# Performance work log

Hardware: AMD Instinct MI355X
Metric: run time of the kernel (lower is better)

The kernel has to match this reference:

```python
import jax, jax.numpy as jnp
import numpy as np

N, C = 8, 3
HD, WD = 1024, 1280   # camera (depth) resolution
HS, WS = 800, 1280    # projector pattern resolution


def _build_calib():
    fx, fy, dx, dy = 1200.0, 1200.0, 640.0, 512.0
    ww = np.arange(WD, dtype=np.float32)[None, :].repeat(HD, 0)
    hh = np.arange(HD, dtype=np.float32)[:, None].repeat(WD, 1)
    vec = np.stack([(ww - dx) / fx, (hh - dy) / fy, np.ones_like(ww)], axis=2)  # [H,W,3]
    th = 0.15
    ext_rot = np.array([[np.cos(th), 0.0, np.sin(th)],
                        [0.0, 1.0, 0.0],
                        [-np.sin(th), 0.0, np.cos(th)]], np.float32)
    abc = np.einsum('ij,hwj->hwi', ext_rot, vec).astype(np.float32)  # [H,W,3]
    abc_mat = np.transpose(abc, (2, 0, 1))  # [3,H,W] (plb.a2t HWC->CHW)
    ext_tran = np.array([200.0, 0.0, 50.0], np.float32)
    pat_intrin = np.array([1100.0, 1100.0, 640.0, 400.0], np.float32)
    return abc_mat, ext_tran, pat_intrin


def setup_inputs() -> dict:
    key = jax.random.key(0)
    k1, k2 = jax.random.split(key)
    abc, tr, pi = _build_calib()
    depth_mat = 500.0 + 500.0 * jax.random.uniform(k1, (N, 1, HD, WD), jnp.float32)
    src_mat = jax.random.normal(k2, (N, C, HS, WS), jnp.float32)
    return {"depth_mat": depth_mat, "src_mat": src_mat,
            "abc_mat": jnp.asarray(abc), "ext_tran": jnp.asarray(tr),
            "pat_intrin": jnp.asarray(pi)}


def _grid_sample_border(src, gx, gy):
    # src: [N,C,Hs,Ws]; gx,gy: [N,H,W] normalized grid; bilinear,
    # align_corners=False, padding_mode='border' (torch semantics).
    n, c, hs, ws = src.shape
    x = ((gx + 1.0) * ws - 1.0) * 0.5
    y = ((gy + 1.0) * hs - 1.0) * 0.5
    x = jnp.clip(x, 0.0, ws - 1.0)
    y = jnp.clip(y, 0.0, hs - 1.0)
    x0 = jnp.floor(x)
    y0 = jnp.floor(y)
    wx = x - x0
    wy = y - y0
    x0i = x0.astype(jnp.int32)
    y0i = y0.astype(jnp.int32)
    x1i = jnp.minimum(x0i + 1, ws - 1)
    y1i = jnp.minimum(y0i + 1, hs - 1)
    b = jnp.arange(n)[:, None, None]

    def g(yi, xi):
        return src[b, :, yi, xi]  # [N,H,W,C]

    out = (g(y0i, x0i) * ((1.0 - wy) * (1.0 - wx))[..., None]
           + g(y0i, x1i) * ((1.0 - wy) * wx)[..., None]
           + g(y1i, x0i) * (wy * (1.0 - wx))[..., None]
           + g(y1i, x1i) * (wy * wx)[..., None])
    return jnp.transpose(out, (0, 3, 1, 2))  # [N,C,H,W]


def reference(depth_mat, src_mat, abc_mat, ext_tran, pat_intrin):
    hs, ws = src_mat.shape[-2:]
    denom = abc_mat[2] * depth_mat + ext_tran[2]          # [N,1,H,W]
    xx = (abc_mat[0] * depth_mat + ext_tran[0]) / denom
    yy = (abc_mat[1] * depth_mat + ext_tran[1]) / denom
    fu, fv, du, dv = pat_intrin
    uu = fu * xx + du
    vv = fv * yy + dv
    # NOTE: original normalizes by (size-1) even with align_corners=False;
    # replicated faithfully.
    gx = 2.0 * uu[:, 0] / (ws - 1) - 1.0                  # [N,H,W]
    gy = 2.0 * vv[:, 0] / (hs - 1) - 1.0
    return _grid_sample_border(src_mat, gx, gy)
```

## Files before the change

### kernel.cpp

```cpp
#include <hip/hip_runtime.h>

#define N_  8
#define C_  3
#define HD_ 1024
#define WD_ 1280
#define HS_ 800
#define WS_ 1280

typedef _Float16 h2_t __attribute__((ext_vector_type(2)));
typedef float f32x4 __attribute__((ext_vector_type(4)));

__device__ __forceinline__ unsigned pack_h2(float a, float b) {
    h2_t h;
    h.x = (_Float16)a;
    h.y = (_Float16)b;
    return __builtin_bit_cast(unsigned, h);
}
__device__ __forceinline__ h2_t as_h2(unsigned u) {
    return __builtin_bit_cast(h2_t, u);
}
__device__ __forceinline__ float fdot2(h2_t a, h2_t b, float c) {
#if __has_builtin(__builtin_amdgcn_fdot2)
    return __builtin_amdgcn_fdot2(a, b, c, false);
#else
    return (float)a.x * (float)b.x + (float)a.y * (float)b.y + c;
#endif
}

__global__ __launch_bounds__(256) void pair_pack_kernel(
    const float* __restrict__ src, uint4* __restrict__ ws)
{
    const size_t HWs = (size_t)HS_ * WS_;
    size_t g = (size_t)blockIdx.x * blockDim.x + threadIdx.x;
    if (g >= (size_t)N_ * HWs) return;
    int n = (int)(g / HWs);
    size_t p = g - (size_t)n * HWs;
    int x = (int)(p % WS_);
    int dx = (x < WS_ - 1) ? 1 : 0;

    const float* s0 = src + (size_t)n * C_ * HWs + p;
    const float* s1 = s0 + HWs;
    const float* s2 = s1 + HWs;

    float c0a = s0[0], c0b = s0[dx];
    float c1a = s1[0], c1b = s1[dx];
    float c2a = s2[0], c2b = s2[dx];

    uint4 e;
    e.x = pack_h2(c0a, c0b);
    e.y = pack_h2(c1a, c1b);
    e.z = pack_h2(c2a, c2b);
    e.w = 0u;
    ws[g] = e;
}

__global__ __launch_bounds__(256) void warp_main4_kernel(
    const float* __restrict__ depth,
    const uint4* __restrict__ wsrc,
    const float* __restrict__ abc,
    const float* __restrict__ tr,
    const float* __restrict__ pin,
    float* __restrict__ out)
{
    const int HW = HD_ * WD_;
    int t = blockIdx.x * blockDim.x + threadIdx.x;
    int base = t * 4;
    if (base >= N_ * HW) return;

    int n  = base / HW;
    int hw = base - n * HW;

    f32x4 d4 = *(const f32x4*)(depth + base);
    f32x4 a4 = *(const f32x4*)(abc + hw);
    f32x4 b4 = *(const f32x4*)(abc + HW + hw);
    f32x4 c4 = *(const f32x4*)(abc + 2 * HW + hw);

    float tx = tr[0], ty = tr[1], tz = tr[2];
    float fu = pin[0], fv = pin[1], du = pin[2], dv = pin[3];

    const size_t HWs = (size_t)HS_ * WS_;
    const uint4* sn = wsrc + (size_t)n * HWs;

    f32x4 r0, r1, r2;

#pragma unroll
    for (int i = 0; i < 4; ++i) {
        float d = d4[i];
        float a = a4[i];
        float b = b4[i];
        float c = c4[i];

        float denom = c * d + tz;
        float inv = 1.0f / denom;
        float xx = (a * d + tx) * inv;
        float yy = (b * d + ty) * inv;
        float uu = fu * xx + du;
        float vv = fv * yy + dv;

        float gx = 2.0f * uu / (float)(WS_ - 1) - 1.0f;
        float gy = 2.0f * vv / (float)(HS_ - 1) - 1.0f;
        float x = ((gx + 1.0f) * (float)WS_ - 1.0f) * 0.5f;
        float y = ((gy + 1.0f) * (float)HS_ - 1.0f) * 0.5f;

        x = fminf(fmaxf(x, 0.0f), (float)(WS_ - 1));
        y = fminf(fmaxf(y, 0.0f), (float)(HS_ - 1));

        float x0f = floorf(x);
        float y0f = floorf(y);
        float wx = x - x0f;
        float wy = y - y0f;
        int x0 = (int)x0f;
        int y0 = (int)y0f;
        int y1 = min(y0 + 1, HS_ - 1);

        uint4 E0 = sn[(size_t)y0 * WS_ + x0];
        uint4 E1 = sn[(size_t)y1 * WS_ + x0];

        float w00 = (1.0f - wy) * (1.0f - wx);
        float w01 = (1.0f - wy) * wx;
        float w10 = wy * (1.0f - wx);
        float w11 = wy * wx;

        h2_t wA = { (_Float16)w00, (_Float16)w01 };
        h2_t wB = { (_Float16)w10, (_Float16)w11 };

        r0[i] = fdot2(as_h2(E0.x), wA, fdot2(as_h2(E1.x), wB, 0.0f));
        r1[i] = fdot2(as_h2(E0.y), wA, fdot2(as_h2(E1.y), wB, 0.0f));
        r2[i] = fdot2(as_h2(E0.z), wA, fdot2(as_h2(E1.z), wB, 0.0f));
    }

    float* on = out + (size_t)n * C_ * HW + hw;
    __builtin_nontemporal_store(r0, (f32x4*)(on));
    __builtin_nontemporal_store(r1, (f32x4*)(on + (size_t)HW));
    __builtin_nontemporal_store(r2, (f32x4*)(on + (size_t)2 * HW));
}

__global__ __launch_bounds__(256) void warp_planar_kernel(
    const float* __restrict__ depth, const float* __restrict__ src,
    const float* __restrict__ abc, const float* __restrict__ tr,
    const float* __restrict__ pin, float* __restrict__ out)
{
    const int HW = HD_ * WD_;
    int idx = blockIdx.x * blockDim.x + threadIdx.x;
    if (idx >= N_ * HW) return;
    int n  = idx / HW;
    int hw = idx - n * HW;
    float d = depth[idx];
    float a = abc[hw];
    float b = abc[HW + hw];
    float c = abc[2 * HW + hw];
    float denom = c * d + tr[2];
    float inv = 1.0f / denom;
    float uu = pin[0] * ((a * d + tr[0]) * inv) + pin[2];
    float vv = pin[1] * ((b * d + tr[1]) * inv) + pin[3];
    float gx = 2.0f * uu / (float)(WS_ - 1) - 1.0f;
    float gy = 2.0f * vv / (float)(HS_ - 1) - 1.0f;
    float x = ((gx + 1.0f) * (float)WS_ - 1.0f) * 0.5f;
    float y = ((gy + 1.0f) * (float)HS_ - 1.0f) * 0.5f;
    x = fminf(fmaxf(x, 0.0f), (float)(WS_ - 1));
    y = fminf(fmaxf(y, 0.0f), (float)(HS_ - 1));
    float x0f = floorf(x), y0f = floorf(y);
    float wx = x - x0f, wy = y - y0f;
    int x0 = (int)x0f, y0 = (int)y0f;
    int x1 = min(x0 + 1, WS_ - 1);
    int y1 = min(y0 + 1, HS_ - 1);
    float w00 = (1.0f - wy) * (1.0f - wx), w01 = (1.0f - wy) * wx;
    float w10 = wy * (1.0f - wx), w11 = wy * wx;
    const size_t HWs = (size_t)HS_ * WS_;
    const float* sn = src + (size_t)n * C_ * HWs;
    int o00 = y0 * WS_ + x0, o01 = y0 * WS_ + x1;
    int o10 = y1 * WS_ + x0, o11 = y1 * WS_ + x1;
    float* on = out + (size_t)n * C_ * HW + hw;
#pragma unroll
    for (int ch = 0; ch < C_; ++ch) {
        const float* sc = sn + (size_t)ch * HWs;
        on[(size_t)ch * HW] = sc[o00] * w00 + sc[o01] * w01
                            + sc[o10] * w10 + sc[o11] * w11;
    }
}

extern "C" void kernel_launch(void* const* d_in, const int* in_sizes, int n_in,
                              void* d_out, int out_size, void* d_ws, size_t ws_size,
                              hipStream_t stream) {
    const float* depth = (const float*)d_in[0];
    const float* src   = (const float*)d_in[1];
    const float* abc   = (const float*)d_in[2];
    const float* tr    = (const float*)d_in[3];
    const float* pin   = (const float*)d_in[4];
    float* out = (float*)d_out;

    const size_t src_px = (size_t)N_ * HS_ * WS_;
    const size_t need = src_px * 16;
    const int total = N_ * HD_ * WD_;
    const int block = 256;

    if (ws_size >= need) {
        const int g1 = (int)((src_px + block - 1) / block);
        pair_pack_kernel<<<g1, block, 0, stream>>>(src, (uint4*)d_ws);
        const int g2 = (total / 4 + block - 1) / block;
        warp_main4_kernel<<<g2, block, 0, stream>>>(depth, (const uint4*)d_ws,
                                                    abc, tr, pin, out);
    } else {
        const int g = (total + block - 1) / block;
        warp_planar_kernel<<<g, block, 0, stream>>>(depth, src, abc, tr, pin, out);
    }
}
```

Measured before the change: 339.4 us.

## Pack source as 8-byte per-pixel fp16 texels and remap blocks across XCDs

```diff
diff --git a/kernel.cpp b/kernel.cpp
--- a/kernel.cpp
+++ b/kernel.cpp
@@ -9,6 +9,7 @@
 
 typedef _Float16 h2_t __attribute__((ext_vector_type(2)));
 typedef float f32x4 __attribute__((ext_vector_type(4)));
+typedef unsigned int uint4_a8 __attribute__((ext_vector_type(4), aligned(8)));
 
 __device__ __forceinline__ unsigned pack_h2(float a, float b) {
     h2_t h;
@@ -19,67 +20,70 @@
 __device__ __forceinline__ h2_t as_h2(unsigned u) {
     return __builtin_bit_cast(h2_t, u);
 }
-__device__ __forceinline__ float fdot2(h2_t a, h2_t b, float c) {
-#if __has_builtin(__builtin_amdgcn_fdot2)
-    return __builtin_amdgcn_fdot2(a, b, c, false);
-#else
-    return (float)a.x * (float)b.x + (float)a.y * (float)b.y + c;
-#endif
-}
-
-__global__ __launch_bounds__(256) void pair_pack_kernel(
-    const float* __restrict__ src, uint4* __restrict__ ws)
+
+__global__ __launch_bounds__(256) void pack_kernel(
+    const float* __restrict__ src, uint2* __restrict__ ws)
 {
     const size_t HWs = (size_t)HS_ * WS_;
-    size_t g = (size_t)blockIdx.x * blockDim.x + threadIdx.x;
-    if (g >= (size_t)N_ * HWs) return;
-    int n = (int)(g / HWs);
-    size_t p = g - (size_t)n * HWs;
-    int x = (int)(p % WS_);
-    int dx = (x < WS_ - 1) ? 1 : 0;
-
-    const float* s0 = src + (size_t)n * C_ * HWs + p;
-    const float* s1 = s0 + HWs;
-    const float* s2 = s1 + HWs;
-
-    float c0a = s0[0], c0b = s0[dx];
-    float c1a = s1[0], c1b = s1[dx];
-    float c2a = s2[0], c2b = s2[dx];
-
-    uint4 e;
-    e.x = pack_h2(c0a, c0b);
-    e.y = pack_h2(c1a, c1b);
-    e.z = pack_h2(c2a, c2b);
-    e.w = 0u;
-    ws[g] = e;
+    size_t t = (size_t)blockIdx.x * blockDim.x + threadIdx.x;
+    size_t base = t * 4;
+    if (base >= (size_t)N_ * HWs) return;
+    int n = (int)(base / HWs);
+    size_t p = base - (size_t)n * HWs;
+    const float* s = src + (size_t)n * C_ * HWs + p;
+
+    f32x4 c0 = __builtin_nontemporal_load((const f32x4*)(s));
+    f32x4 c1 = __builtin_nontemporal_load((const f32x4*)(s + HWs));
+    f32x4 c2 = __builtin_nontemporal_load((const f32x4*)(s + 2 * HWs));
+
+    uint4 A, B;
+    A.x = pack_h2(c0[0], c1[0]);
+    A.y = pack_h2(c2[0], 0.0f);
+    A.z = pack_h2(c0[1], c1[1]);
+    A.w = pack_h2(c2[1], 0.0f);
+    B.x = pack_h2(c0[2], c1[2]);
+    B.y = pack_h2(c2[2], 0.0f);
+    B.z = pack_h2(c0[3], c1[3]);
+    B.w = pack_h2(c2[3], 0.0f);
+
+    uint4* o = (uint4*)(ws + base);
+    o[0] = A;
+    o[1] = B;
 }
 
 __global__ __launch_bounds__(256) void warp_main4_kernel(
     const float* __restrict__ depth,
-    const uint4* __restrict__ wsrc,
+    const uint2* __restrict__ wsrc,
     const float* __restrict__ abc,
     const float* __restrict__ tr,
     const float* __restrict__ pin,
     float* __restrict__ out)
 {
     const int HW = HD_ * WD_;
-    int t = blockIdx.x * blockDim.x + threadIdx.x;
+
+    int bid = blockIdx.x;
+    if ((gridDim.x & 7) == 0) {
+        int per = gridDim.x >> 3;
+        bid = (bid & 7) * per + (bid >> 3);
+    }
+
+    int t = bid * blockDim.x + threadIdx.x;
     int base = t * 4;
     if (base >= N_ * HW) return;
 
     int n  = base / HW;
     int hw = base - n * HW;
 
-    f32x4 d4 = *(const f32x4*)(depth + base);
-    f32x4 a4 = *(const f32x4*)(abc + hw);
-    f32x4 b4 = *(const f32x4*)(abc + HW + hw);
-    f32x4 c4 = *(const f32x4*)(abc + 2 * HW + hw);
+    f32x4 d4 = __builtin_nontemporal_load((const f32x4*)(depth + base));
+    f32x4 a4 = __builtin_nontemporal_load((const f32x4*)(abc + hw));
+    f32x4 b4 = __builtin_nontemporal_load((const f32x4*)(abc + HW + hw));
+    f32x4 c4 = __builtin_nontemporal_load((const f32x4*)(abc + 2 * HW + hw));
 
     float tx = tr[0], ty = tr[1], tz = tr[2];
     float fu = pin[0], fv = pin[1], du = pin[2], dv = pin[3];
 
     const size_t HWs = (size_t)HS_ * WS_;
-    const uint4* sn = wsrc + (size_t)n * HWs;
+    const uint2* sn = wsrc + (size_t)n * HWs;
 
     f32x4 r0, r1, r2;
 
@@ -107,26 +111,39 @@
 
         float x0f = floorf(x);
         float y0f = floorf(y);
-        float wx = x - x0f;
-        float wy = y - y0f;
         int x0 = (int)x0f;
         int y0 = (int)y0f;
         int y1 = min(y0 + 1, HS_ - 1);
 
-        uint4 E0 = sn[(size_t)y0 * WS_ + x0];
-        uint4 E1 = sn[(size_t)y1 * WS_ + x0];
-
-        float w00 = (1.0f - wy) * (1.0f - wx);
-        float w01 = (1.0f - wy) * wx;
-        float w10 = wy * (1.0f - wx);
-        float w11 = wy * wx;
-
-        h2_t wA = { (_Float16)w00, (_Float16)w01 };
-        h2_t wB = { (_Float16)w10, (_Float16)w11 };
-
-        r0[i] = fdot2(as_h2(E0.x), wA, fdot2(as_h2(E1.x), wB, 0.0f));
-        r1[i] = fdot2(as_h2(E0.y), wA, fdot2(as_h2(E1.y), wB, 0.0f));
-        r2[i] = fdot2(as_h2(E0.z), wA, fdot2(as_h2(E1.z), wB, 0.0f));
+        int xa = min(x0, WS_ - 2);
+        float wx = (x - x0f) + (float)(x0 - xa);
+        float wy = y - y0f;
+
+        uint4_a8 E0 = *(const uint4_a8*)(sn + (size_t)y0 * WS_ + xa);
+        uint4_a8 E1 = *(const uint4_a8*)(sn + (size_t)y1 * WS_ + xa);
+
+        h2_t p0a = as_h2(E0.x);
+        h2_t p0b = as_h2(E0.y);
+        h2_t p0c = as_h2(E0.z);
+        h2_t p0d = as_h2(E0.w);
+        h2_t p1a = as_h2(E1.x);
+        h2_t p1b = as_h2(E1.y);
+        h2_t p1c = as_h2(E1.z);
+        h2_t p1d = as_h2(E1.w);
+
+        float iwx = 1.0f - wx;
+        float iwy = 1.0f - wy;
+
+        float t0c0 = iwx * (float)p0a.x + wx * (float)p0c.x;
+        float t0c1 = iwx * (float)p0a.y + wx * (float)p0c.y;
+        float t0c2 = iwx * (float)p0b.x + wx * (float)p0d.x;
+        float t1c0 = iwx * (float)p1a.x + wx * (float)p1c.x;
+        float t1c1 = iwx * (float)p1a.y + wx * (float)p1c.y;
+        float t1c2 = iwx * (float)p1b.x + wx * (float)p1d.x;
+
+        r0[i] = iwy * t0c0 + wy * t1c0;
+        r1[i] = iwy * t0c1 + wy * t1c1;
+        r2[i] = iwy * t0c2 + wy * t1c2;
     }
 
     float* on = out + (size_t)n * C_ * HW + hw;
@@ -190,15 +207,15 @@
     float* out = (float*)d_out;
 
     const size_t src_px = (size_t)N_ * HS_ * WS_;
-    const size_t need = src_px * 16;
+    const size_t need = src_px * 8;
     const int total = N_ * HD_ * WD_;
     const int block = 256;
 
     if (ws_size >= need) {
-        const int g1 = (int)((src_px + block - 1) / block);
-        pair_pack_kernel<<<g1, block, 0, stream>>>(src, (uint4*)d_ws);
+        const int g1 = (int)((src_px / 4 + block - 1) / block);
+        pack_kernel<<<g1, block, 0, stream>>>(src, (uint2*)d_ws);
         const int g2 = (total / 4 + block - 1) / block;
-        warp_main4_kernel<<<g2, block, 0, stream>>>(depth, (const uint4*)d_ws,
+        warp_main4_kernel<<<g2, block, 0, stream>>>(depth, (const uint2*)d_ws,
                                                     abc, tr, pin, out);
     } else {
         const int g = (total + block - 1) / block;
```

Result: faster. 328.8 us (-3.1%).

## Vectorize pair-pack, use one pixel per thread with XCD-aware block remap

Applied to the files above, without the earlier changes.

```diff
diff --git a/kernel.cpp b/kernel.cpp
--- a/kernel.cpp
+++ b/kernel.cpp
@@ -31,30 +31,40 @@
     const float* __restrict__ src, uint4* __restrict__ ws)
 {
     const size_t HWs = (size_t)HS_ * WS_;
-    size_t g = (size_t)blockIdx.x * blockDim.x + threadIdx.x;
-    if (g >= (size_t)N_ * HWs) return;
-    int n = (int)(g / HWs);
-    size_t p = g - (size_t)n * HWs;
+    size_t t = (size_t)blockIdx.x * blockDim.x + threadIdx.x;
+    size_t base = t * 4;
+    if (base >= (size_t)N_ * HWs) return;
+    int n = (int)(base / HWs);
+    size_t p = base - (size_t)n * HWs;
     int x = (int)(p % WS_);
-    int dx = (x < WS_ - 1) ? 1 : 0;
 
     const float* s0 = src + (size_t)n * C_ * HWs + p;
     const float* s1 = s0 + HWs;
     const float* s2 = s1 + HWs;
 
-    float c0a = s0[0], c0b = s0[dx];
-    float c1a = s1[0], c1b = s1[dx];
-    float c2a = s2[0], c2b = s2[dx];
-
-    uint4 e;
-    e.x = pack_h2(c0a, c0b);
-    e.y = pack_h2(c1a, c1b);
-    e.z = pack_h2(c2a, c2b);
-    e.w = 0u;
-    ws[g] = e;
-}
-
-__global__ __launch_bounds__(256) void warp_main4_kernel(
+    f32x4 c0 = *(const f32x4*)s0;
+    f32x4 c1 = *(const f32x4*)s1;
+    f32x4 c2 = *(const f32x4*)s2;
+    int nxt = (x + 4 < WS_) ? 4 : 3;
+    float e0 = s0[nxt], e1 = s1[nxt], e2 = s2[nxt];
+
+    float c0v[5] = { c0[0], c0[1], c0[2], c0[3], e0 };
+    float c1v[5] = { c1[0], c1[1], c1[2], c1[3], e1 };
+    float c2v[5] = { c2[0], c2[1], c2[2], c2[3], e2 };
+
+    uint4* o = ws + base;
+#pragma unroll
+    for (int j = 0; j < 4; ++j) {
+        uint4 e;
+        e.x = pack_h2(c0v[j], c0v[j + 1]);
+        e.y = pack_h2(c1v[j], c1v[j + 1]);
+        e.z = pack_h2(c2v[j], c2v[j + 1]);
+        e.w = 0u;
+        o[j] = e;
+    }
+}
+
+__global__ __launch_bounds__(256) void warp_main_kernel(
     const float* __restrict__ depth,
     const uint4* __restrict__ wsrc,
     const float* __restrict__ abc,
@@ -63,76 +73,67 @@
     float* __restrict__ out)
 {
     const int HW = HD_ * WD_;
-    int t = blockIdx.x * blockDim.x + threadIdx.x;
-    int base = t * 4;
-    if (base >= N_ * HW) return;
-
-    int n  = base / HW;
-    int hw = base - n * HW;
-
-    f32x4 d4 = *(const f32x4*)(depth + base);
-    f32x4 a4 = *(const f32x4*)(abc + hw);
-    f32x4 b4 = *(const f32x4*)(abc + HW + hw);
-    f32x4 c4 = *(const f32x4*)(abc + 2 * HW + hw);
+
+    int bid = blockIdx.x;
+    if ((gridDim.x & 7) == 0) {
+        int per = gridDim.x >> 3;
+        bid = (bid & 7) * per + (bid >> 3);
+    }
+
+    int idx = bid * blockDim.x + threadIdx.x;
+    if (idx >= N_ * HW) return;
+
+    int n  = idx / HW;
+    int hw = idx - n * HW;
+
+    float d = depth[idx];
+    float a = abc[hw];
+    float b = abc[HW + hw];
+    float c = abc[2 * HW + hw];
 
     float tx = tr[0], ty = tr[1], tz = tr[2];
     float fu = pin[0], fv = pin[1], du = pin[2], dv = pin[3];
 
+    float denom = c * d + tz;
+    float inv = 1.0f / denom;
+    float xx = (a * d + tx) * inv;
+    float yy = (b * d + ty) * inv;
+    float uu = fu * xx + du;
+    float vv = fv * yy + dv;
+
+    float gx = 2.0f * uu / (float)(WS_ - 1) - 1.0f;
+    float gy = 2.0f * vv / (float)(HS_ - 1) - 1.0f;
+    float x = ((gx + 1.0f) * (float)WS_ - 1.0f) * 0.5f;
+    float y = ((gy + 1.0f) * (float)HS_ - 1.0f) * 0.5f;
+
+    x = fminf(fmaxf(x, 0.0f), (float)(WS_ - 1));
+    y = fminf(fmaxf(y, 0.0f), (float)(HS_ - 1));
+
+    float x0f = floorf(x);
+    float y0f = floorf(y);
+    float wx = x - x0f;
+    float wy = y - y0f;
+    int x0 = (int)x0f;
+    int y0 = (int)y0f;
+    int y1 = min(y0 + 1, HS_ - 1);
+
     const size_t HWs = (size_t)HS_ * WS_;
     const uint4* sn = wsrc + (size_t)n * HWs;
 
-    f32x4 r0, r1, r2;
-
-#pragma unroll
-    for (int i = 0; i < 4; ++i) {
-        float d = d4[i];
-        float a = a4[i];
-        float b = b4[i];
-        float c = c4[i];
-
-        float denom = c * d + tz;
-        float inv = 1.0f / denom;
-        float xx = (a * d + tx) * inv;
-        float yy = (b * d + ty) * inv;
-        float uu = fu * xx + du;
-        float vv = fv * yy + dv;
-
-        float gx = 2.0f * uu / (float)(WS_ - 1) - 1.0f;
-        float gy = 2.0f * vv / (float)(HS_ - 1) - 1.0f;
-        float x = ((gx + 1.0f) * (float)WS_ - 1.0f) * 0.5f;
-        float y = ((gy + 1.0f) * (float)HS_ - 1.0f) * 0.5f;
-
-        x = fminf(fmaxf(x, 0.0f), (float)(WS_ - 1));
-        y = fminf(fmaxf(y, 0.0f), (float)(HS_ - 1));
-
-        float x0f = floorf(x);
-        float y0f = floorf(y);
-        float wx = x - x0f;
-        float wy = y - y0f;
-        int x0 = (int)x0f;
-        int y0 = (int)y0f;
-        int y1 = min(y0 + 1, HS_ - 1);
-
-        uint4 E0 = sn[(size_t)y0 * WS_ + x0];
-        uint4 E1 = sn[(size_t)y1 * WS_ + x0];
-
-        float w00 = (1.0f - wy) * (1.0f - wx);
-        float w01 = (1.0f - wy) * wx;
-        float w10 = wy * (1.0f - wx);
-        float w11 = wy * wx;
-
-        h2_t wA = { (_Float16)w00, (_Float16)w01 };
-        h2_t wB = { (_Float16)w10, (_Float16)w11 };
-
-        r0[i] = fdot2(as_h2(E0.x), wA, fdot2(as_h2(E1.x), wB, 0.0f));
-        r1[i] = fdot2(as_h2(E0.y), wA, fdot2(as_h2(E1.y), wB, 0.0f));
-        r2[i] = fdot2(as_h2(E0.z), wA, fdot2(as_h2(E1.z), wB, 0.0f));
-    }
+    uint4 E0 = sn[(size_t)y0 * WS_ + x0];
+    uint4 E1 = sn[(size_t)y1 * WS_ + x0];
+
+    h2_t wA = { (_Float16)(1.0f - wx), (_Float16)wx };
+    float iwy = 1.0f - wy;
+
+    float v0 = iwy * fdot2(as_h2(E0.x), wA, 0.0f) + wy * fdot2(as_h2(E1.x), wA, 0.0f);
+    float v1 = iwy * fdot2(as_h2(E0.y), wA, 0.0f) + wy * fdot2(as_h2(E1.y), wA, 0.0f);
+    float v2 = iwy * fdot2(as_h2(E0.z), wA, 0.0f) + wy * fdot2(as_h2(E1.z), wA, 0.0f);
 
     float* on = out + (size_t)n * C_ * HW + hw;
-    __builtin_nontemporal_store(r0, (f32x4*)(on));
-    __builtin_nontemporal_store(r1, (f32x4*)(on + (size_t)HW));
-    __builtin_nontemporal_store(r2, (f32x4*)(on + (size_t)2 * HW));
+    __builtin_nontemporal_store(v0, on);
+    __builtin_nontemporal_store(v1, on + (size_t)HW);
+    __builtin_nontemporal_store(v2, on + (size_t)2 * HW);
 }
 
 __global__ __launch_bounds__(256) void warp_planar_kernel(
@@ -195,11 +196,11 @@
     const int block = 256;
 
     if (ws_size >= need) {
-        const int g1 = (int)((src_px + block - 1) / block);
+        const int g1 = (int)((src_px / 4 + block - 1) / block);
         pair_pack_kernel<<<g1, block, 0, stream>>>(src, (uint4*)d_ws);
-        const int g2 = (total / 4 + block - 1) / block;
-        warp_main4_kernel<<<g2, block, 0, stream>>>(depth, (const uint4*)d_ws,
-                                                    abc, tr, pin, out);
+        const int g2 = (total + block - 1) / block;
+        warp_main_kernel<<<g2, block, 0, stream>>>(depth, (const uint4*)d_ws,
+                                                   abc, tr, pin, out);
     } else {
         const int g = (total + block - 1) / block;
         warp_planar_kernel<<<g, block, 0, stream>>>(depth, src, abc, tr, pin, out);
```

Result: no change. 340.7 us (+0.4%).
